# Kernel optimization log

Hardware: AMD Instinct MI355X
Metric: run time of the kernel (lower is better)

The kernel has to match this reference:

```python
import jax, jax.numpy as jnp
import numpy as np
from jax import lax

WS = 8          # window size
HEADS = 8
DIM = 192       # embed_dim == v_dim inside block
HD = DIM // HEADS
SCALE = HD ** -0.5
EPS = 1e-5


def _rel_pos_index(ws):
    coords = np.stack(np.meshgrid(np.arange(ws), np.arange(ws), indexing='ij'))  # (2,ws,ws)
    cf = coords.reshape(2, -1)                       # (2, n)
    rel = (cf[:, :, None] - cf[:, None, :]).transpose(1, 2, 0).astype(np.int64)  # (n,n,2)
    rel[..., 0] += ws - 1
    rel[..., 1] += ws - 1
    rel[..., 0] *= 2 * ws - 1
    return rel.sum(-1)                               # (n, n) int


def _ln(x, w, b):
    m = jnp.mean(x, axis=-1, keepdims=True)
    v = jnp.mean(jnp.square(x - m), axis=-1, keepdims=True)
    return (x - m) * lax.rsqrt(v + EPS) * w + b


def _conv3x3(x, w, b):
    y = lax.conv_general_dilated(x, w, (1, 1), ((1, 1), (1, 1)),
                                 dimension_numbers=('NCHW', 'OIHW', 'NCHW'))
    return y + b[None, :, None, None]


def setup_inputs():
    key = jax.random.key(0)
    ks = jax.random.split(key, 24)
    f = lambda k, shape: (jax.random.normal(k, shape, jnp.float32) * 0.02)
    inp = {
        'x': jax.random.normal(ks[0], (8, 96, 128, 128), jnp.float32),
        'v': jax.random.normal(ks[1], (8, 96, 128, 128), jnp.float32),
        'pq_w': f(ks[2], (DIM, 96, 3, 3)), 'pq_b': f(ks[3], (DIM,)),
        'pv_w': f(ks[4], (DIM, 96, 3, 3)), 'pv_b': f(ks[5], (DIM,)),
        'n1_w': jnp.ones((DIM,)), 'n1_b': jnp.zeros((DIM,)),
        'n2_w': jnp.ones((DIM,)), 'n2_b': jnp.zeros((DIM,)),
        'n3_w': jnp.ones((DIM,)), 'n3_b': jnp.zeros((DIM,)),
        'n4_w': jnp.ones((DIM,)), 'n4_b': jnp.zeros((DIM,)),
        'q_w': f(ks[6], (DIM, DIM)),
        'kv_w': f(ks[7], (2 * DIM, DIM)),
        'ap_w': f(ks[8], (DIM, DIM)), 'ap_b': f(ks[9], (DIM,)),
        'rpb': f(ks[10], ((2 * WS - 1) * (2 * WS - 1), HEADS)),
        'fc1_w': f(ks[11], (4 * DIM, DIM)), 'fc1_b': f(ks[12], (4 * DIM,)),
        'fc2_w': f(ks[13], (DIM, 4 * DIM)), 'fc2_b': f(ks[14], (DIM,)),
    }
    return inp


def reference(x, v, pq_w, pq_b, pv_w, pv_b, n1_w, n1_b, n2_w, n2_b, n3_w, n3_b,
              n4_w, n4_b, q_w, kv_w, ap_w, ap_b, rpb, fc1_w, fc1_b, fc2_w, fc2_b):
    # conv projections (input_dim != embed_dim, v_dim != embed_dim)
    x = _conv3x3(x, pq_w, pq_b)
    v = _conv3x3(v, pv_w, pv_b)
    x_proj, v_proj = x, v
    b, c, h, w = x.shape
    n = WS * WS

    xs = _ln(x.reshape(b, c, h * w).transpose(0, 2, 1), n1_w, n1_b).reshape(b, h, w, c)
    vs = _ln(v.reshape(b, c, h * w).transpose(0, 2, 1), n2_w, n2_b).reshape(b, h, w, c)

    pad_r = (WS - w % WS) % WS
    pad_b_ = (WS - h % WS) % WS
    if pad_r or pad_b_:
        xs = jnp.pad(xs, ((0, 0), (0, pad_b_), (0, pad_r), (0, 0)))
        vs = jnp.pad(vs, ((0, 0), (0, pad_b_), (0, pad_r), (0, 0)))
    hp, wp = h + pad_b_, w + pad_r

    def partition(t):  # (b,hp,wp,c) -> (nw, n, c)
        t = t.reshape(b, hp // WS, WS, wp // WS, WS, c)
        return t.transpose(0, 1, 3, 2, 4, 5).reshape(-1, n, c)

    xw = partition(xs)
    vw = partition(vs)

    # cross-window attention
    q = (xw @ q_w.T).reshape(-1, n, HEADS, HD).transpose(0, 2, 1, 3) * SCALE  # (nw,H,n,hd)
    kv = (vw @ kv_w.T).reshape(-1, n, 2, HEADS, HD).transpose(2, 0, 3, 1, 4)
    k, vv = kv[0], kv[1]                                                     # (nw,H,n,hd)
    attn = jnp.einsum('whqd,whkd->whqk', q, k)
    rel_idx = _rel_pos_index(WS)                                             # static (n,n)
    bias = rpb[rel_idx.reshape(-1)].reshape(n, n, HEADS).transpose(2, 0, 1)  # (H,n,n)
    attn = jax.nn.softmax(attn + bias[None], axis=-1)
    out = jnp.einsum('whqk,whkd->whqd', attn, vv).transpose(0, 2, 1, 3).reshape(-1, n, c)
    out = out @ ap_w.T + ap_b                                                # (nw,n,c)

    # window reverse + crop
    out = out.reshape(b, hp // WS, wp // WS, WS, WS, c).transpose(0, 1, 3, 2, 4, 5)
    out = out.reshape(b, hp, wp, c)[:, :h, :w, :].reshape(b, h * w, c)

    # mlp: note original does x = mlp(norm3(x)); x = x + drop_path(x) -> 2*mlp_out
    m = _ln(out, n3_w, n3_b)
    m = jax.nn.gelu(m @ fc1_w.T + fc1_b, approximate=False) @ fc2_w.T + fc2_b
    m = m + m
    m = _ln(m, n4_w, n4_b)
    m = m.reshape(b, h, w, c).transpose(0, 3, 1, 2)
    return m + x_proj + v_proj
```

## Files before the change

### kernel.cpp

```cpp
#include <hip/hip_runtime.h>
#include <hip/hip_bf16.h>
#include <math.h>

typedef _Float16 f16;
typedef _Float16 half8 __attribute__((ext_vector_type(8)));
typedef float f32x4 __attribute__((ext_vector_type(4)));

#define IMG 128
#define CIN 96
#define CH  192
#define SCALE_Q 0.2041241452319315f

__device__ __forceinline__ f32x4 mfma16(half8 a, half8 b, f32x4 c) {
  return __builtin_amdgcn_mfma_f32_16x16x32_f16(a, b, c, 0, 0, 0);
}

template <bool WH>
__device__ __forceinline__ half8 loadW(const void* W, int row, int k, int ldk) {
  if constexpr (WH) {
    return *(const half8*)((const f16*)W + (size_t)row * ldk + k);
  } else {
    const float* p = (const float*)W + (size_t)row * ldk + k;
    const float4 a = *(const float4*)p;
    const float4 b = *(const float4*)(p + 4);
    half8 h;
    h[0] = (f16)a.x; h[1] = (f16)a.y; h[2] = (f16)a.z; h[3] = (f16)a.w;
    h[4] = (f16)b.x; h[5] = (f16)b.y; h[6] = (f16)b.z; h[7] = (f16)b.w;
    return h;
  }
}

__device__ __forceinline__ float gelu(float x) {
  const float u = 0.70710678118654752f * x;
  const float a = fabsf(u);
  const float t = __builtin_amdgcn_rcpf(1.0f + 0.3275911f * a);
  const float poly = t * (0.254829592f + t * (-0.284496736f +
                     t * (1.421413741f + t * (-1.453152027f + t * 1.061405429f))));
  float er = 1.0f - poly * __expf(-u * u);
  er = (u < 0.f) ? -er : er;
  return 0.5f * x * (1.0f + er);
}

__global__ __launch_bounds__(256) void reorder_w(
    const float* __restrict__ pq_w, const float* __restrict__ pv_w,
    const float* __restrict__ qW, const float* __restrict__ kvW,
    f16* __restrict__ Wr, f16* __restrict__ wq16) {
  const int i = blockIdx.x * 256 + threadIdx.x;
  if (i < 2 * 192 * 864) {
    const int which = i / (192 * 864);
    const int rem = i - which * (192 * 864);
    const int co = rem / 864;
    const int kk = rem - co * 864;
    const int s = kk / 96;
    const int ci = kk - s * 96;
    const float* src = which ? pv_w : pq_w;
    Wr[i] = (f16)src[co * 864 + ci * 9 + s];
  } else if (wq16) {
    const int j = i - 2 * 192 * 864;
    if (j < 110592)
      wq16[j] = (f16)(j < 36864 ? qW[j] : kvW[j - 36864]);
  }
}

__global__ __launch_bounds__(256) void reorder_w2(
    const float* __restrict__ apW, const float* __restrict__ w1,
    const float* __restrict__ w2, f16* __restrict__ dst) {
  const int i = blockIdx.x * 256 + threadIdx.x;
  if (i >= 331776) return;
  float v;
  if (i < 36864)       v = apW[i];
  else if (i < 184320) v = w1[i - 36864];
  else                 v = w2[i - 184320];
  dst[i] = (f16)v;
}

__global__ __launch_bounds__(256, 2) void conv3x3_mfma(
    const float* __restrict__ xin, const float* __restrict__ vin,
    const f16* __restrict__ Wr,
    const float* __restrict__ pq_b, const float* __restrict__ pv_b,
    f16* __restrict__ xp, f16* __restrict__ vp) {
  int bz = blockIdx.x;
  const int which = bz >> 10; bz &= 1023;
  const int b = bz >> 7;
  const int yp = (bz >> 1) & 63;
  const int xseg = bz & 1;
  const int y0 = yp * 2;
  const int x0 = xseg * 64;
  const float* in = which ? vin : xin;
  const float* bias = which ? pv_b : pq_b;
  const f16* W = Wr + (size_t)which * 192 * 864;
  f16* out = which ? vp : xp;

  __shared__ __align__(16) f16 ST[4 * 66 * 104];
  const int tid = threadIdx.x;
  #pragma unroll
  for (int batch = 0; batch < 9; ++batch) {
    float vals[11];
    bool oks[11];
    int sts[11];
    #pragma unroll
    for (int u = 0; u < 11; ++u) {
      const int i = tid + (batch * 11 + u) * 256;
      const int r = i / 6336;
      const int rem2 = i - r * 6336;
      const int c = rem2 / 66;
      const int xx = rem2 - c * 66;
      const int gy = y0 + r - 1;
      const int gx = x0 - 1 + xx;
      oks[u] = ((unsigned)gy < IMG) && ((unsigned)gx < IMG);
      const int cgy = min(max(gy, 0), IMG - 1);
      const int cgx = min(max(gx, 0), IMG - 1);
      vals[u] = in[(((size_t)b * CIN + c) * IMG + cgy) * IMG + cgx];
      sts[u] = (r * 66 + xx) * 104 + c;
    }
    #pragma unroll
    for (int u = 0; u < 11; ++u)
      ST[sts[u]] = oks[u] ? (f16)vals[u] : (f16)0.f;
  }
  __syncthreads();

  const int lane = tid & 63;
  const int wv = tid >> 6;
  const int l15 = lane & 15;
  const int quad = lane >> 4;
  const int nb = wv * 48;

  f32x4 acc[8][3];
  #pragma unroll
  for (int mt = 0; mt < 8; ++mt)
    #pragma unroll
    for (int j = 0; j < 3; ++j) acc[mt][j] = (f32x4)0.f;

  #pragma unroll
  for (int s = 0; s < 9; ++s) {
    const int ky = s / 3, kx = s - ky * 3;
    #pragma unroll
    for (int kstep = 0; kstep < 3; ++kstep) {
      const int k = kstep * 32 + quad * 8;
      half8 a[8];
      #pragma unroll
      for (int mt = 0; mt < 8; ++mt)
        a[mt] = *(const half8*)(ST + (((mt >> 2) + ky) * 66 + (mt & 3) * 16 + l15 + kx) * 104 + k);
      #pragma unroll
      for (int j = 0; j < 3; ++j) {
        const half8 bf = *(const half8*)(W + (size_t)(nb + j * 16 + l15) * 864 + s * 96 + k);
        #pragma unroll
        for (int mt = 0; mt < 8; ++mt) acc[mt][j] = mfma16(a[mt], bf, acc[mt][j]);
      }
    }
  }
  __syncthreads();

  #pragma unroll
  for (int j = 0; j < 3; ++j) {
    const int n = nb + j * 16 + l15;
    const float bn = bias[n];
    #pragma unroll
    for (int mt = 0; mt < 8; ++mt) {
      const int lt = (mt >> 2) * 64 + (mt & 3) * 16 + quad * 4;
      #pragma unroll
      for (int reg = 0; reg < 4; ++reg)
        ST[(lt + reg) * 204 + n] = (f16)(acc[mt][j][reg] + bn);
    }
  }
  __syncthreads();

  const size_t rowbase0 = ((size_t)(b * IMG + y0) * IMG + x0) * CH;
  const size_t rowbase1 = ((size_t)(b * IMG + y0 + 1) * IMG + x0) * CH;
  #pragma unroll
  for (int it = 0; it < 12; ++it) {
    const int i = tid + it * 256;
    const int tok = i / 24, c8 = i - tok * 24;
    const half8 hval = *(const half8*)(ST + tok * 204 + c8 * 8);
    const int trow = tok >> 6, tx = tok & 63;
    f16* dst = out + (trow ? rowbase1 : rowbase0) + (size_t)tx * CH + c8 * 8;
    *(half8*)dst = hval;
  }
}

template <bool WH>
__global__ __launch_bounds__(256, 1) void ln_qkv_mfma(
    f16* __restrict__ xp, const f16* __restrict__ vp,
    const float* __restrict__ n1w, const float* __restrict__ n1b,
    const float* __restrict__ n2w, const float* __restrict__ n2b,
    const void* __restrict__ qW, const void* __restrict__ kvW,
    f16* __restrict__ qb, f16* __restrict__ kb, f16* __restrict__ vb) {
  const int tid = threadIdx.x;
  const int lane = tid & 63;
  const int wv = tid >> 6;
  const int l15 = lane & 15;
  const int quad = lane >> 4;
  const int tok0 = blockIdx.x * 32;
  __shared__ __align__(16) f16 U[32 * 588];
  f16* Ax = U;
  f16* Av = U + 6400;

  {
    const int r = tid >> 3;
    const int s = tid & 7;
    const size_t gbase = (size_t)(tok0 + r) * 192 + s * 24;
    half8 hx[3], hv[3];
    const half8* px = (const half8*)(xp + gbase);
    const half8* pv = (const half8*)(vp + gbase);
    #pragma unroll
    for (int i = 0; i < 3; ++i) { hx[i] = px[i]; hv[i] = pv[i]; }
    float xv[24], vvv[24];
    float sx = 0.f, sx2 = 0.f, sv = 0.f, sv2 = 0.f;
    #pragma unroll
    for (int i = 0; i < 24; ++i) {
      xv[i] = (float)hx[i >> 3][i & 7];
      vvv[i] = (float)hv[i >> 3][i & 7];
      sx += xv[i]; sx2 += xv[i] * xv[i];
      sv += vvv[i]; sv2 += vvv[i] * vvv[i];
    }
    half8 hr[3];
    #pragma unroll
    for (int i = 0; i < 24; ++i) hr[i >> 3][i & 7] = (f16)(xv[i] + vvv[i]);
    half8* pr = (half8*)(xp + gbase);
    #pragma unroll
    for (int i = 0; i < 3; ++i) pr[i] = hr[i];
    #pragma unroll
    for (int m = 1; m < 8; m <<= 1) {
      sx += __shfl_xor(sx, m, 64); sx2 += __shfl_xor(sx2, m, 64);
      sv += __shfl_xor(sv, m, 64); sv2 += __shfl_xor(sv2, m, 64);
    }
    const float mx = sx * (1.f / 192.f);
    const float rx = rsqrtf(sx2 * (1.f / 192.f) - mx * mx + 1e-5f);
    const float mv = sv * (1.f / 192.f);
    const float rv = rsqrtf(sv2 * (1.f / 192.f) - mv * mv + 1e-5f);
    #pragma unroll
    for (int i = 0; i < 24; ++i) {
      const int c = s * 24 + i;
      Ax[r * 200 + c] = (f16)((xv[i] - mx) * rx * n1w[c] + n1b[c]);
      Av[r * 200 + c] = (f16)((vvv[i] - mv) * rv * n2w[c] + n2b[c]);
    }
  }
  __syncthreads();

  const int nb = wv * 144;
  f32x4 acc[2][9];
  #pragma unroll
  for (int mt = 0; mt < 2; ++mt)
    #pragma unroll
    for (int j = 0; j < 9; ++j) acc[mt][j] = (f32x4)0.f;

  for (int kc = 0; kc < 6; ++kc) {
    const int k = kc * 32 + quad * 8;
    half8 wb[9];
    #pragma unroll
    for (int j = 0; j < 9; ++j) {
      const int n0 = nb + j * 16;
      if (n0 < 192) wb[j] = loadW<WH>(qW, n0 + l15, k, 192);
      else          wb[j] = loadW<WH>(kvW, n0 - 192 + l15, k, 192);
    }
    const half8 ax0 = *(const half8*)(Ax + l15 * 200 + k);
    const half8 ax1 = *(const half8*)(Ax + (16 + l15) * 200 + k);
    const half8 av0 = *(const half8*)(Av + l15 * 200 + k);
    const half8 av1 = *(const half8*)(Av + (16 + l15) * 200 + k);
    #pragma unroll
    for (int j = 0; j < 9; ++j) {
      const int n0 = nb + j * 16;
      if (n0 < 192) {
        acc[0][j] = mfma16(ax0, wb[j], acc[0][j]);
        acc[1][j] = mfma16(ax1, wb[j], acc[1][j]);
      } else {
        acc[0][j] = mfma16(av0, wb[j], acc[0][j]);
        acc[1][j] = mfma16(av1, wb[j], acc[1][j]);
      }
    }
  }
  __syncthreads();

  #pragma unroll
  for (int j = 0; j < 9; ++j) {
    const int n = nb + j * 16 + l15;
    const float scale = (n < 192) ? SCALE_Q : 1.f;
    #pragma unroll
    for (int mt = 0; mt < 2; ++mt)
      #pragma unroll
      for (int reg = 0; reg < 4; ++reg) {
        const int r = mt * 16 + quad * 4 + reg;
        U[r * 588 + n] = (f16)(acc[mt][j][reg] * scale);
      }
  }
  __syncthreads();

  const int yrow = (tok0 >> 7) & 127;
  const int bb = tok0 >> 14;
  const int x0b = tok0 & 127;
  const int wib = bb * 256 + ((yrow >> 3) << 4) + (x0b >> 3);
  const int trow = (yrow & 7) * 8;
  f16* const bufs[3] = {qb, kb, vb};
  #pragma unroll
  for (int it = 0; it < 9; ++it) {
    const int i = tid + it * 256;
    const int c24 = i % 24;
    const int g = i / 24;
    const int h = g & 7;
    const int g2 = g >> 3;
    const int wloc = g2 & 3;
    const int buf = g2 >> 2;
    const int t8 = c24 / 3, c3 = c24 - t8 * 3;
    const int r = wloc * 8 + t8;
    const half8 hval = *(const half8*)(U + r * 588 + buf * 192 + h * 24 + c3 * 8);
    f16* dst = bufs[buf] + (size_t)(wib + wloc) * 12288 + (trow + t8) * 24 + h * 1536 + c3 * 8;
    *(half8*)dst = hval;
  }
}

__global__ __launch_bounds__(64) void attn64(
    const f16* __restrict__ qb, const f16* __restrict__ kb,
    const f16* __restrict__ vb, const float* __restrict__ rpb,
    f16* __restrict__ fb) {
  const int wh = blockIdx.x;
  const int h = wh & 7;
  const int w = wh >> 3;
  const int t = threadIdx.x;
  __shared__ __align__(16) float ks[64 * 24];
  __shared__ __align__(16) float vs[64 * 24];
  __shared__ float bsh[225];
  const f16* kbase = kb + (size_t)wh * 1536;
  const f16* vbase = vb + (size_t)wh * 1536;
  for (int i = t; i < 1536; i += 64) { ks[i] = (float)kbase[i]; vs[i] = (float)vbase[i]; }
  for (int i = t; i < 225; i += 64) bsh[i] = rpb[i * 8 + h];
  float q[24];
  const f16* qrow = qb + ((size_t)wh * 64 + t) * 24;
  #pragma unroll
  for (int d = 0; d < 24; ++d) q[d] = (float)qrow[d];
  __syncthreads();
  const int qy = t >> 3, qx = t & 7;
  float s[64];
  float mx = -1e30f;
  #pragma unroll
  for (int kk = 0; kk < 64; ++kk) {
    float acc = 0.f;
    #pragma unroll
    for (int d = 0; d < 24; ++d) acc += q[d] * ks[kk * 24 + d];
    const int ky = kk >> 3, kx = kk & 7;
    acc += bsh[(qy - ky + 7) * 15 + (qx - kx + 7)];
    s[kk] = acc;
    mx = fmaxf(mx, acc);
  }
  float sum = 0.f;
  #pragma unroll
  for (int kk = 0; kk < 64; ++kk) { const float e = __expf(s[kk] - mx); s[kk] = e; sum += e; }
  const float inv = 1.0f / sum;
  float o[24];
  #pragma unroll
  for (int d = 0; d < 24; ++d) o[d] = 0.f;
  #pragma unroll
  for (int kk = 0; kk < 64; ++kk) {
    const float p = s[kk];
    #pragma unroll
    for (int d = 0; d < 24; ++d) o[d] += p * vs[kk * 24 + d];
  }
  f16* orow = fb + ((size_t)w * 64 + t) * 192 + h * 24;
  #pragma unroll
  for (int d = 0; d < 24; ++d) orow[d] = (f16)(o[d] * inv);
}

__global__ __launch_bounds__(256, 2) void ap_mlp_mfma(
    const f16* __restrict__ fb, const f16* __restrict__ apW,
    const float* __restrict__ apb,
    const float* __restrict__ n3w, const float* __restrict__ n3b,
    const f16* __restrict__ w1, const float* __restrict__ b1,
    const f16* __restrict__ w2, const float* __restrict__ b2,
    const float* __restrict__ n4w, const float* __restrict__ n4b,
    const f16* __restrict__ res, float* __restrict__ out) {
  const int tid = threadIdx.x;
  const int lane = tid & 63;
  const int wv = tid >> 6;
  const int l15 = lane & 15;
  const int quad = lane >> 4;
  const int wt0 = blockIdx.x * 32;
  __shared__ __align__(16) f16 SB[32 * 776];
  __shared__ float rs3[32], rq3[32], rs4[32], rq4[32];
  if (tid < 32) { rs3[tid] = 0.f; rq3[tid] = 0.f; rs4[tid] = 0.f; rq4[tid] = 0.f; }
  for (int i = tid; i < 32 * 24; i += 256) {
    const int r = i / 24, s = i - r * 24;
    *(half8*)(SB + r * 200 + s * 8) = *(const half8*)(fb + (size_t)(wt0 + r) * 192 + s * 8);
  }
  __syncthreads();

  const int nbp = wv * 48;
  int cc[3]; float apbv[3], w3v[3], b3v[3];
  #pragma unroll
  for (int j = 0; j < 3; ++j) {
    cc[j] = nbp + j * 16 + l15;
    apbv[j] = apb[cc[j]]; w3v[j] = n3w[cc[j]]; b3v[j] = n3b[cc[j]];
  }
  const int nb1 = wv * 192;
  float b1v[12];
  #pragma unroll
  for (int j = 0; j < 12; ++j) b1v[j] = b1[nb1 + j * 16 + l15];

  f32x4 accp[2][3];
  #pragma unroll
  for (int mt = 0; mt < 2; ++mt)
    #pragma unroll
    for (int j = 0; j < 3; ++j) accp[mt][j] = (f32x4)0.f;
  #pragma unroll
  for (int g = 0; g < 2; ++g) {
    half8 wb[3][3];
    #pragma unroll
    for (int u = 0; u < 3; ++u) {
      const int k = (g * 3 + u) * 32 + quad * 8;
      #pragma unroll
      for (int j = 0; j < 3; ++j)
        wb[u][j] = *(const half8*)(apW + (size_t)cc[j] * 192 + k);
    }
    #pragma unroll
    for (int u = 0; u < 3; ++u) {
      const int k = (g * 3 + u) * 32 + quad * 8;
      const half8 a0 = *(const half8*)(SB + l15 * 200 + k);
      const half8 a1 = *(const half8*)(SB + (16 + l15) * 200 + k);
      #pragma unroll
      for (int j = 0; j < 3; ++j) {
        accp[0][j] = mfma16(a0, wb[u][j], accp[0][j]);
        accp[1][j] = mfma16(a1, wb[u][j], accp[1][j]);
      }
    }
  }
  #pragma unroll
  for (int mt = 0; mt < 2; ++mt)
    #pragma unroll
    for (int j = 0; j < 3; ++j)
      #pragma unroll
      for (int reg = 0; reg < 4; ++reg) accp[mt][j][reg] += apbv[j];

  {
    float ssum[8], ssq[8];
    #pragma unroll
    for (int mt = 0; mt < 2; ++mt)
      #pragma unroll
      for (int reg = 0; reg < 4; ++reg) {
        const int i = mt * 4 + reg;
        const float a0 = accp[mt][0][reg], a1 = accp[mt][1][reg], a2 = accp[mt][2][reg];
        ssum[i] = a0 + a1 + a2;
        ssq[i] = a0 * a0 + a1 * a1 + a2 * a2;
      }
    #pragma unroll
    for (int mm = 1; mm < 16; mm <<= 1)
      #pragma unroll
      for (int i = 0; i < 8; ++i) {
        ssum[i] += __shfl_xor(ssum[i], mm, 64);
        ssq[i] += __shfl_xor(ssq[i], mm, 64);
      }
    if (l15 == 0) {
      #pragma unroll
      for (int mt = 0; mt < 2; ++mt)
        #pragma unroll
        for (int reg = 0; reg < 4; ++reg) {
          const int row = mt * 16 + quad * 4 + reg;
          atomicAdd(&rs3[row], ssum[mt * 4 + reg]);
          atomicAdd(&rq3[row], ssq[mt * 4 + reg]);
        }
    }
  }
  __syncthreads();
  #pragma unroll
  for (int mt = 0; mt < 2; ++mt)
    #pragma unroll
    for (int reg = 0; reg < 4; ++reg) {
      const int row = mt * 16 + quad * 4 + reg;
      const float mean = rs3[row] * (1.f / 192.f);
      const float rstd = rsqrtf(rq3[row] * (1.f / 192.f) - mean * mean + 1e-5f);
      #pragma unroll
      for (int j = 0; j < 3; ++j)
        SB[row * 200 + cc[j]] = (f16)((accp[mt][j][reg] - mean) * rstd * w3v[j] + b3v[j]);
    }
  __syncthreads();

  f32x4 acc1[2][12];
  #pragma unroll
  for (int mt = 0; mt < 2; ++mt)
    #pragma unroll
    for (int j = 0; j < 12; ++j) acc1[mt][j] = (f32x4)0.f;
  for (int kc = 0; kc < 6; ++kc) {
    const int k = kc * 32 + quad * 8;
    half8 wb[12];
    #pragma unroll
    for (int j = 0; j < 12; ++j)
      wb[j] = *(const half8*)(w1 + (size_t)(nb1 + j * 16 + l15) * 192 + k);
    const half8 a0 = *(const half8*)(SB + l15 * 200 + k);
    const half8 a1 = *(const half8*)(SB + (16 + l15) * 200 + k);
    #pragma unroll
    for (int j = 0; j < 12; ++j) {
      acc1[0][j] = mfma16(a0, wb[j], acc1[0][j]);
      acc1[1][j] = mfma16(a1, wb[j], acc1[1][j]);
    }
  }
  __syncthreads();
  #pragma unroll
  for (int j = 0; j < 12; ++j) {
    const int n = nb1 + j * 16 + l15;
    #pragma unroll
    for (int mt = 0; mt < 2; ++mt)
      #pragma unroll
      for (int reg = 0; reg < 4; ++reg) {
        const int row = mt * 16 + quad * 4 + reg;
        SB[row * 776 + n] = (f16)gelu(acc1[mt][j][reg] + b1v[j]);
      }
  }
  __syncthreads();

  const int wi = wt0 >> 6;
  const int t_base = wt0 & 63;
  const int b_img = wi >> 8;
  const int wy = (wi >> 4) & 15;
  const int wx = wi & 15;
  float rr[2][3][4];
  #pragma unroll
  for (int mt = 0; mt < 2; ++mt) {
    const int t0 = t_base + mt * 16 + quad * 4;
    const int y = wy * 8 + (t0 >> 3);
    const int xx0 = wx * 8 + (t0 & 7);
    const size_t tokbase = ((size_t)(b_img * 128 + y)) * 128 + xx0;
    #pragma unroll
    for (int j = 0; j < 3; ++j)
      #pragma unroll
      for (int reg = 0; reg < 4; ++reg)
        rr[mt][j][reg] = (float)res[(tokbase + reg) * 192 + cc[j]];
  }

  f32x4 acc2[2][3];
  #pragma unroll
  for (int mt = 0; mt < 2; ++mt)
    #pragma unroll
    for (int j = 0; j < 3; ++j) acc2[mt][j] = (f32x4)0.f;
  for (int g = 0; g < 6; ++g) {
    half8 wb[4][3];
    #pragma unroll
    for (int u = 0; u < 4; ++u) {
      const int k = (g * 4 + u) * 32 + quad * 8;
      #pragma unroll
      for (int j = 0; j < 3; ++j)
        wb[u][j] = *(const half8*)(w2 + (size_t)cc[j] * 768 + k);
    }
    #pragma unroll
    for (int u = 0; u < 4; ++u) {
      const int k = (g * 4 + u) * 32 + quad * 8;
      const half8 a0 = *(const half8*)(SB + l15 * 776 + k);
      const half8 a1 = *(const half8*)(SB + (16 + l15) * 776 + k);
      #pragma unroll
      for (int j = 0; j < 3; ++j) {
        acc2[0][j] = mfma16(a0, wb[u][j], acc2[0][j]);
        acc2[1][j] = mfma16(a1, wb[u][j], acc2[1][j]);
      }
    }
  }
  float w4[3], b4[3];
  #pragma unroll
  for (int j = 0; j < 3; ++j) {
    const float bj = b2[cc[j]];
    w4[j] = n4w[cc[j]]; b4[j] = n4b[cc[j]];
    #pragma unroll
    for (int mt = 0; mt < 2; ++mt)
      #pragma unroll
      for (int reg = 0; reg < 4; ++reg)
        acc2[mt][j][reg] = 2.f * (acc2[mt][j][reg] + bj);
  }
  float ssum[8], ssq[8];
  #pragma unroll
  for (int mt = 0; mt < 2; ++mt)
    #pragma unroll
    for (int reg = 0; reg < 4; ++reg) {
      const int i = mt * 4 + reg;
      const float a0 = acc2[mt][0][reg], a1 = acc2[mt][1][reg], a2 = acc2[mt][2][reg];
      ssum[i] = a0 + a1 + a2;
      ssq[i] = a0 * a0 + a1 * a1 + a2 * a2;
    }
  #pragma unroll
  for (int mm = 1; mm < 16; mm <<= 1)
    #pragma unroll
    for (int i = 0; i < 8; ++i) {
      ssum[i] += __shfl_xor(ssum[i], mm, 64);
      ssq[i] += __shfl_xor(ssq[i], mm, 64);
    }
  if (l15 == 0) {
    #pragma unroll
    for (int mt = 0; mt < 2; ++mt)
      #pragma unroll
      for (int reg = 0; reg < 4; ++reg) {
        const int row = mt * 16 + quad * 4 + reg;
        atomicAdd(&rs4[row], ssum[mt * 4 + reg]);
        atomicAdd(&rq4[row], ssq[mt * 4 + reg]);
      }
  }
  __syncthreads();

  #pragma unroll
  for (int mt = 0; mt < 2; ++mt) {
    const int row0 = mt * 16 + quad * 4;
    const int t0 = t_base + row0;
    const int y = wy * 8 + (t0 >> 3);
    const int x0 = wx * 8 + (t0 & 7);
    float mean[4], rstd[4];
    #pragma unroll
    for (int reg = 0; reg < 4; ++reg) {
      const int row = row0 + reg;
      mean[reg] = rs4[row] * (1.f / 192.f);
      rstd[reg] = rsqrtf(rq4[row] * (1.f / 192.f) - mean[reg] * mean[reg] + 1e-5f);
    }
    #pragma unroll
    for (int j = 0; j < 3; ++j) {
      float4 o;
      float vals[4];
      #pragma unroll
      for (int reg = 0; reg < 4; ++reg)
        vals[reg] = (acc2[mt][j][reg] - mean[reg]) * rstd[reg] * w4[j] + b4[j] + rr[mt][j][reg];
      o.x = vals[0]; o.y = vals[1]; o.z = vals[2]; o.w = vals[3];
      float* dst = out + ((size_t)(b_img * 192 + cc[j])) * 16384 + (y * 128 + x0);
      *(float4*)dst = o;
    }
  }
}

extern "C" void kernel_launch(void* const* d_in, const int* in_sizes, int n_in,
                              void* d_out, int out_size, void* d_ws, size_t ws_size,
                              hipStream_t stream) {
  (void)in_sizes; (void)n_in; (void)out_size;
  const float* x    = (const float*)d_in[0];
  const float* v    = (const float*)d_in[1];
  const float* pq_w = (const float*)d_in[2];
  const float* pq_b = (const float*)d_in[3];
  const float* pv_w = (const float*)d_in[4];
  const float* pv_b = (const float*)d_in[5];
  const float* n1w  = (const float*)d_in[6];
  const float* n1b  = (const float*)d_in[7];
  const float* n2w  = (const float*)d_in[8];
  const float* n2b  = (const float*)d_in[9];
  const float* n3w  = (const float*)d_in[10];
  const float* n3b  = (const float*)d_in[11];
  const float* n4w  = (const float*)d_in[12];
  const float* n4b  = (const float*)d_in[13];
  const float* qW   = (const float*)d_in[14];
  const float* kvW  = (const float*)d_in[15];
  const float* apW  = (const float*)d_in[16];
  const float* apb  = (const float*)d_in[17];
  const float* rpb  = (const float*)d_in[18];
  const float* w1   = (const float*)d_in[19];
  const float* b1   = (const float*)d_in[20];
  const float* w2   = (const float*)d_in[21];
  const float* b2   = (const float*)d_in[22];
  float* out = (float*)d_out;

  const size_t HE = 25165824;
  f16* xp   = (f16*)d_ws;
  f16* vp   = xp + HE;
  f16* vvb  = vp + HE;
  f16* qb   = (f16*)d_out;
  f16* kb   = qb + HE;
  f16* fb   = vp;
  f16* Wr   = vvb;
  f16* wtail = vvb + HE;
  const bool big = ws_size >= (3 * HE + 110592) * sizeof(f16);

  reorder_w<<<big ? 1728 : 1296, 256, 0, stream>>>(pq_w, pv_w, qW, kvW, Wr,
                                                   big ? wtail : (f16*)nullptr);
  conv3x3_mfma<<<2048, 256, 0, stream>>>(x, v, Wr, pq_b, pv_b, xp, vp);
  if (big)
    ln_qkv_mfma<true><<<4096, 256, 0, stream>>>(xp, vp, n1w, n1b, n2w, n2b,
                                                wtail, wtail + 36864, qb, kb, vvb);
  else
    ln_qkv_mfma<false><<<4096, 256, 0, stream>>>(xp, vp, n1w, n1b, n2w, n2b,
                                                 qW, kvW, qb, kb, vvb);
  attn64<<<16384, 64, 0, stream>>>(qb, kb, vvb, rpb, fb);
  reorder_w2<<<1296, 256, 0, stream>>>(apW, w1, w2, vvb);
  ap_mlp_mfma<<<4096, 256, 0, stream>>>(fb, vvb, apb, n3w, n3b,
                                        vvb + 36864, b1, vvb + 184320, b2,
                                        n4w, n4b, xp, out);
}
```

Before: 1.031 ms.

## Vectorize conv/attn input loads and double-buffer weight fetches in GEMM loops

The conv input staging now loads float4 rows per channel instead of scalar gathers with divisions. Attention loads K, V and Q as half8 vectors. The QKV, fc1 and fc2 GEMM loops double-buffer weight registers so the next k-chunk is prefetched while the current one runs on MFMA, and the attn-proj weights are preloaded before the barrier. This should reduce global load latency stalls and instruction count, at the cost of higher register pressure, which may lower occupancy.

Result: slower. 1.088 ms (+5.5%).

```diff
diff --git a/kernel.cpp b/kernel.cpp
--- a/kernel.cpp
+++ b/kernel.cpp
@@ -93,29 +93,39 @@
 
   __shared__ __align__(16) f16 ST[4 * 66 * 104];
   const int tid = threadIdx.x;
-  #pragma unroll
-  for (int batch = 0; batch < 9; ++batch) {
-    float vals[11];
-    bool oks[11];
-    int sts[11];
-    #pragma unroll
-    for (int u = 0; u < 11; ++u) {
-      const int i = tid + (batch * 11 + u) * 256;
-      const int r = i / 6336;
-      const int rem2 = i - r * 6336;
-      const int c = rem2 / 66;
-      const int xx = rem2 - c * 66;
+  {
+    const int hf = tid & 1;
+    #pragma unroll
+    for (int t3 = 0; t3 < 3; ++t3) {
+      const int pr = (tid >> 1) + t3 * 128;
+      const int r = pr / 96;
+      const int c = pr - r * 96;
       const int gy = y0 + r - 1;
-      const int gx = x0 - 1 + xx;
-      oks[u] = ((unsigned)gy < IMG) && ((unsigned)gx < IMG);
+      const bool rowok = ((unsigned)gy < IMG);
       const int cgy = min(max(gy, 0), IMG - 1);
-      const int cgx = min(max(gx, 0), IMG - 1);
-      vals[u] = in[(((size_t)b * CIN + c) * IMG + cgy) * IMG + cgx];
-      sts[u] = (r * 66 + xx) * 104 + c;
-    }
-    #pragma unroll
-    for (int u = 0; u < 11; ++u)
-      ST[sts[u]] = oks[u] ? (f16)vals[u] : (f16)0.f;
+      const float* src = in + (((size_t)b * CIN + c) * IMG + cgy) * IMG;
+      float4 v4[9];
+      #pragma unroll
+      for (int u = 0; u < 9; ++u) {
+        const int gx0 = x0 - 4 + (hf * 9 + u) * 4;
+        const int gxc = min(max(gx0, 0), IMG - 4);
+        v4[u] = *(const float4*)(src + gxc);
+      }
+      f16* drow = ST + r * 66 * 104 + c;
+      #pragma unroll
+      for (int u = 0; u < 9; ++u) {
+        const float* pv = (const float*)&v4[u];
+        #pragma unroll
+        for (int e = 0; e < 4; ++e) {
+          const int xx = (hf * 9 + u) * 4 + e - 3;
+          if (xx >= 0 && xx < 66) {
+            const int gx = x0 - 1 + xx;
+            const bool ok = rowok && ((unsigned)gx < IMG);
+            drow[xx * 104] = ok ? (f16)pv[e] : (f16)0.f;
+          }
+        }
+      }
+    }
   }
   __syncthreads();
 
@@ -244,14 +254,26 @@
     #pragma unroll
     for (int j = 0; j < 9; ++j) acc[mt][j] = (f32x4)0.f;
 
+  half8 wA[9], wB[9];
+  #pragma unroll
+  for (int j = 0; j < 9; ++j) {
+    const int n0 = nb + j * 16;
+    if (n0 < 192) wA[j] = loadW<WH>(qW, n0 + l15, quad * 8, 192);
+    else          wA[j] = loadW<WH>(kvW, n0 - 192 + l15, quad * 8, 192);
+  }
+  #pragma unroll
   for (int kc = 0; kc < 6; ++kc) {
     const int k = kc * 32 + quad * 8;
-    half8 wb[9];
-    #pragma unroll
-    for (int j = 0; j < 9; ++j) {
-      const int n0 = nb + j * 16;
-      if (n0 < 192) wb[j] = loadW<WH>(qW, n0 + l15, k, 192);
-      else          wb[j] = loadW<WH>(kvW, n0 - 192 + l15, k, 192);
+    if (kc < 5) {
+      const int k2 = k + 32;
+      #pragma unroll
+      for (int j = 0; j < 9; ++j) {
+        const int n0 = nb + j * 16;
+        half8 w;
+        if (n0 < 192) w = loadW<WH>(qW, n0 + l15, k2, 192);
+        else          w = loadW<WH>(kvW, n0 - 192 + l15, k2, 192);
+        if ((kc & 1) == 0) wB[j] = w; else wA[j] = w;
+      }
     }
     const half8 ax0 = *(const half8*)(Ax + l15 * 200 + k);
     const half8 ax1 = *(const half8*)(Ax + (16 + l15) * 200 + k);
@@ -259,13 +281,14 @@
     const half8 av1 = *(const half8*)(Av + (16 + l15) * 200 + k);
     #pragma unroll
     for (int j = 0; j < 9; ++j) {
+      const half8 w = ((kc & 1) == 0) ? wA[j] : wB[j];
       const int n0 = nb + j * 16;
       if (n0 < 192) {
-        acc[0][j] = mfma16(ax0, wb[j], acc[0][j]);
-        acc[1][j] = mfma16(ax1, wb[j], acc[1][j]);
+        acc[0][j] = mfma16(ax0, w, acc[0][j]);
+        acc[1][j] = mfma16(ax1, w, acc[1][j]);
       } else {
-        acc[0][j] = mfma16(av0, wb[j], acc[0][j]);
-        acc[1][j] = mfma16(av1, wb[j], acc[1][j]);
+        acc[0][j] = mfma16(av0, w, acc[0][j]);
+        acc[1][j] = mfma16(av1, w, acc[1][j]);
       }
     }
   }
@@ -321,12 +344,27 @@
   __shared__ float bsh[225];
   const f16* kbase = kb + (size_t)wh * 1536;
   const f16* vbase = vb + (size_t)wh * 1536;
-  for (int i = t; i < 1536; i += 64) { ks[i] = (float)kbase[i]; vs[i] = (float)vbase[i]; }
+  #pragma unroll
+  for (int it = 0; it < 3; ++it) {
+    const int i = t + it * 64;
+    const half8 hk = *(const half8*)(kbase + (size_t)i * 8);
+    const half8 hv = *(const half8*)(vbase + (size_t)i * 8);
+    #pragma unroll
+    for (int e = 0; e < 8; ++e) {
+      ks[i * 8 + e] = (float)hk[e];
+      vs[i * 8 + e] = (float)hv[e];
+    }
+  }
   for (int i = t; i < 225; i += 64) bsh[i] = rpb[i * 8 + h];
   float q[24];
-  const f16* qrow = qb + ((size_t)wh * 64 + t) * 24;
-  #pragma unroll
-  for (int d = 0; d < 24; ++d) q[d] = (float)qrow[d];
+  {
+    const half8* qrow = (const half8*)(qb + ((size_t)wh * 64 + t) * 24);
+    half8 hq[3];
+    #pragma unroll
+    for (int i = 0; i < 3; ++i) hq[i] = qrow[i];
+    #pragma unroll
+    for (int d = 0; d < 24; ++d) q[d] = (float)hq[d >> 3][d & 7];
+  }
   __syncthreads();
   const int qy = t >> 3, qx = t & 7;
   float s[64];
@@ -380,7 +418,6 @@
     const int r = i / 24, s = i - r * 24;
     *(half8*)(SB + r * 200 + s * 8) = *(const half8*)(fb + (size_t)(wt0 + r) * 192 + s * 8);
   }
-  __syncthreads();
 
   const int nbp = wv * 48;
   int cc[3]; float apbv[3], w3v[3], b3v[3];
@@ -389,10 +426,19 @@
     cc[j] = nbp + j * 16 + l15;
     apbv[j] = apb[cc[j]]; w3v[j] = n3w[cc[j]]; b3v[j] = n3b[cc[j]];
   }
+  half8 wp[6][3];
+  #pragma unroll
+  for (int u6 = 0; u6 < 6; ++u6) {
+    const int k = u6 * 32 + quad * 8;
+    #pragma unroll
+    for (int j = 0; j < 3; ++j)
+      wp[u6][j] = *(const half8*)(apW + (size_t)cc[j] * 192 + k);
+  }
   const int nb1 = wv * 192;
   float b1v[12];
   #pragma unroll
   for (int j = 0; j < 12; ++j) b1v[j] = b1[nb1 + j * 16 + l15];
+  __syncthreads();
 
   f32x4 accp[2][3];
   #pragma unroll
@@ -400,25 +446,14 @@
     #pragma unroll
     for (int j = 0; j < 3; ++j) accp[mt][j] = (f32x4)0.f;
   #pragma unroll
-  for (int g = 0; g < 2; ++g) {
-    half8 wb[3][3];
-    #pragma unroll
-    for (int u = 0; u < 3; ++u) {
-      const int k = (g * 3 + u) * 32 + quad * 8;
-      #pragma unroll
-      for (int j = 0; j < 3; ++j)
-        wb[u][j] = *(const half8*)(apW + (size_t)cc[j] * 192 + k);
-    }
-    #pragma unroll
-    for (int u = 0; u < 3; ++u) {
-      const int k = (g * 3 + u) * 32 + quad * 8;
-      const half8 a0 = *(const half8*)(SB + l15 * 200 + k);
-      const half8 a1 = *(const half8*)(SB + (16 + l15) * 200 + k);
-      #pragma unroll
-      for (int j = 0; j < 3; ++j) {
-        accp[0][j] = mfma16(a0, wb[u][j], accp[0][j]);
-        accp[1][j] = mfma16(a1, wb[u][j], accp[1][j]);
-      }
+  for (int u6 = 0; u6 < 6; ++u6) {
+    const int k = u6 * 32 + quad * 8;
+    const half8 a0 = *(const half8*)(SB + l15 * 200 + k);
+    const half8 a1 = *(const half8*)(SB + (16 + l15) * 200 + k);
+    #pragma unroll
+    for (int j = 0; j < 3; ++j) {
+      accp[0][j] = mfma16(a0, wp[u6][j], accp[0][j]);
+      accp[1][j] = mfma16(a1, wp[u6][j], accp[1][j]);
     }
   }
   #pragma unroll
@@ -476,18 +511,30 @@
   for (int mt = 0; mt < 2; ++mt)
     #pragma unroll
     for (int j = 0; j < 12; ++j) acc1[mt][j] = (f32x4)0.f;
-  for (int kc = 0; kc < 6; ++kc) {
-    const int k = kc * 32 + quad * 8;
-    half8 wb[12];
+  {
+    half8 wA[12], wB[12];
     #pragma unroll
     for (int j = 0; j < 12; ++j)
-      wb[j] = *(const half8*)(w1 + (size_t)(nb1 + j * 16 + l15) * 192 + k);
-    const half8 a0 = *(const half8*)(SB + l15 * 200 + k);
-    const half8 a1 = *(const half8*)(SB + (16 + l15) * 200 + k);
-    #pragma unroll
-    for (int j = 0; j < 12; ++j) {
-      acc1[0][j] = mfma16(a0, wb[j], acc1[0][j]);
-      acc1[1][j] = mfma16(a1, wb[j], acc1[1][j]);
+      wA[j] = *(const half8*)(w1 + (size_t)(nb1 + j * 16 + l15) * 192 + quad * 8);
+    #pragma unroll
+    for (int kc = 0; kc < 6; ++kc) {
+      const int k = kc * 32 + quad * 8;
+      if (kc < 5) {
+        const int k2 = k + 32;
+        #pragma unroll
+        for (int j = 0; j < 12; ++j) {
+          const half8 w = *(const half8*)(w1 + (size_t)(nb1 + j * 16 + l15) * 192 + k2);
+          if ((kc & 1) == 0) wB[j] = w; else wA[j] = w;
+        }
+      }
+      const half8 a0 = *(const half8*)(SB + l15 * 200 + k);
+      const half8 a1 = *(const half8*)(SB + (16 + l15) * 200 + k);
+      #pragma unroll
+      for (int j = 0; j < 12; ++j) {
+        const half8 w = ((kc & 1) == 0) ? wA[j] : wB[j];
+        acc1[0][j] = mfma16(a0, w, acc1[0][j]);
+        acc1[1][j] = mfma16(a1, w, acc1[1][j]);
+      }
     }
   }
   __syncthreads();
@@ -528,24 +575,39 @@
   for (int mt = 0; mt < 2; ++mt)
     #pragma unroll
     for (int j = 0; j < 3; ++j) acc2[mt][j] = (f32x4)0.f;
-  for (int g = 0; g < 6; ++g) {
-    half8 wb[4][3];
+  {
+    half8 wA[4][3], wB[4][3];
     #pragma unroll
     for (int u = 0; u < 4; ++u) {
-      const int k = (g * 4 + u) * 32 + quad * 8;
+      const int k = u * 32 + quad * 8;
       #pragma unroll
       for (int j = 0; j < 3; ++j)
-        wb[u][j] = *(const half8*)(w2 + (size_t)cc[j] * 768 + k);
-    }
-    #pragma unroll
-    for (int u = 0; u < 4; ++u) {
-      const int k = (g * 4 + u) * 32 + quad * 8;
-      const half8 a0 = *(const half8*)(SB + l15 * 776 + k);
-      const half8 a1 = *(const half8*)(SB + (16 + l15) * 776 + k);
-      #pragma unroll
-      for (int j = 0; j < 3; ++j) {
-        acc2[0][j] = mfma16(a0, wb[u][j], acc2[0][j]);
-        acc2[1][j] = mfma16(a1, wb[u][j], acc2[1][j]);
+        wA[u][j] = *(const half8*)(w2 + (size_t)cc[j] * 768 + k);
+    }
+    #pragma unroll
+    for (int g = 0; g < 6; ++g) {
+      if (g < 5) {
+        #pragma unroll
+        for (int u = 0; u < 4; ++u) {
+          const int k2 = ((g + 1) * 4 + u) * 32 + quad * 8;
+          #pragma unroll
+          for (int j = 0; j < 3; ++j) {
+            const half8 w = *(const half8*)(w2 + (size_t)cc[j] * 768 + k2);
+            if ((g & 1) == 0) wB[u][j] = w; else wA[u][j] = w;
+          }
+        }
+      }
+      #pragma unroll
+      for (int u = 0; u < 4; ++u) {
+        const int k = (g * 4 + u) * 32 + quad * 8;
+        const half8 a0 = *(const half8*)(SB + l15 * 776 + k);
+        const half8 a1 = *(const half8*)(SB + (16 + l15) * 776 + k);
+        #pragma unroll
+        for (int j = 0; j < 3; ++j) {
+          const half8 w = ((g & 1) == 0) ? wA[u][j] : wB[u][j];
+          acc2[0][j] = mfma16(a0, w, acc2[0][j]);
+          acc2[1][j] = mfma16(a1, w, acc2[1][j]);
+        }
       }
     }
   }
```
